# Kernel tuning notes

Measured on AMD Instinct MI355X. Metric: run time of the kernel, lower is better.

Reference implementation:

```python
import jax, jax.numpy as jnp
import numpy as np

B, N = 128, 1024


def setup_inputs() -> dict:
    key = jax.random.key(0)
    k1, k2 = jax.random.split(key)
    vector = jax.random.uniform(k1, (B, N), dtype=jnp.float32)
    interactions = jax.random.normal(k2, (N, N), dtype=jnp.float32)
    return {"vector": vector, "interactions": interactions}


def reference(vector, interactions):
    # x: [B,1,N], y: [B,N,1] -> broadcast dirac delta [B,N,N]
    x = vector[:, None, :]
    y = vector[:, :, None]
    dd = (1.0 - x) * (1.0 - y) + x * y  # [B,N,N]
    dd = jnp.triu(dd)                   # keep upper triangle incl. diagonal
    energy = dd * interactions          # [B,N,N] * [N,N] broadcast
    return energy.reshape(vector.shape[0], -1).sum(axis=1)  # [B]
```

## Files before the change

### kernel.cpp

```cpp
#include <hip/hip_runtime.h>

#define NDIM 1024
#define BDIM 128
#define TS 32
#define NT (NDIM / TS)
#define NTILES (NT * (NT + 1) / 2)

__global__ __launch_bounds__(128) void potts_zero(float* __restrict__ out) {
    out[threadIdx.x] = 0.0f;
}

__global__ __launch_bounds__(256) void potts_tile(
    const float* __restrict__ V,
    const float* __restrict__ W,
    float* __restrict__ out)
{
    const int t = blockIdx.x;
    int ti = 0, rem = t;
    while (rem >= NT - ti) { rem -= NT - ti; ++ti; }
    const int tj = ti + rem;
    const int I0 = ti * TS, J0 = tj * TS;
    const bool diag = (ti == tj);

    __shared__ float wt[TS][36];
    __shared__ float rs[TS];
    __shared__ float red[4][BDIM];

    const int tid = threadIdx.x;
    const int w = tid >> 6;
    const int l = tid & 63;
    const int b0 = l, b1 = l + 64;

    {
        const int r = tid >> 3, c4 = (tid & 7) * 4;
        float4 w4 = *(const float4*)(W + (size_t)(I0 + r) * NDIM + (J0 + c4));
        if (diag) {
            if (c4 + 0 < r) w4.x = 0.0f;
            if (c4 + 1 < r) w4.y = 0.0f;
            if (c4 + 2 < r) w4.z = 0.0f;
            if (c4 + 3 < r) w4.w = 0.0f;
        }
        *(float4*)(&wt[r][c4]) = w4;
        float rsum = (w4.x + w4.y) + (w4.z + w4.w);
        rsum += __shfl_xor(rsum, 1);
        rsum += __shfl_xor(rsum, 2);
        rsum += __shfl_xor(rsum, 4);
        if ((tid & 7) == 0) rs[r] = rsum;
    }

    float4 vj0[8], vj1[8];
    {
        const float* p0 = V + (size_t)b0 * NDIM + J0;
        const float* p1 = V + (size_t)b1 * NDIM + J0;
#pragma unroll
        for (int j4 = 0; j4 < 8; ++j4) {
            vj0[j4] = *(const float4*)(p0 + 4 * j4);
            vj1[j4] = *(const float4*)(p1 + 4 * j4);
        }
    }
    float q0[8], r0[8], q1[8], r1[8];
    {
        const float* p0 = V + (size_t)b0 * NDIM + I0 + w * 8;
        const float* p1 = V + (size_t)b1 * NDIM + I0 + w * 8;
        const float4 a0 = *(const float4*)(p0), a1 = *(const float4*)(p0 + 4);
        const float4 c0 = *(const float4*)(p1), c1 = *(const float4*)(p1 + 4);
        const float va[8] = {a0.x, a0.y, a0.z, a0.w, a1.x, a1.y, a1.z, a1.w};
        const float vc[8] = {c0.x, c0.y, c0.z, c0.w, c1.x, c1.y, c1.z, c1.w};
#pragma unroll
        for (int k = 0; k < 8; ++k) {
            q0[k] = 1.0f - va[k]; r0[k] = 2.0f * va[k] - 1.0f;
            q1[k] = 1.0f - vc[k]; r1[k] = 2.0f * vc[k] - 1.0f;
        }
    }

    __syncthreads();

    float acc0 = 0.0f, acc1 = 0.0f;
#pragma unroll
    for (int k = 0; k < 8; ++k) {
        const float* wrow = &wt[w * 8 + k][0];
        float pa0 = 0.f, pb0 = 0.f, pa1 = 0.f, pb1 = 0.f;
#pragma unroll
        for (int j4 = 0; j4 < 8; j4 += 2) {
            const float4 wa = *(const float4*)(wrow + 4 * j4);
            const float4 wb = *(const float4*)(wrow + 4 * j4 + 4);
            pa0 = fmaf(wa.x, vj0[j4].x, pa0);
            pa0 = fmaf(wa.y, vj0[j4].y, pa0);
            pa0 = fmaf(wa.z, vj0[j4].z, pa0);
            pa0 = fmaf(wa.w, vj0[j4].w, pa0);
            pa1 = fmaf(wa.x, vj1[j4].x, pa1);
            pa1 = fmaf(wa.y, vj1[j4].y, pa1);
            pa1 = fmaf(wa.z, vj1[j4].z, pa1);
            pa1 = fmaf(wa.w, vj1[j4].w, pa1);
            pb0 = fmaf(wb.x, vj0[j4 + 1].x, pb0);
            pb0 = fmaf(wb.y, vj0[j4 + 1].y, pb0);
            pb0 = fmaf(wb.z, vj0[j4 + 1].z, pb0);
            pb0 = fmaf(wb.w, vj0[j4 + 1].w, pb0);
            pb1 = fmaf(wb.x, vj1[j4 + 1].x, pb1);
            pb1 = fmaf(wb.y, vj1[j4 + 1].y, pb1);
            pb1 = fmaf(wb.z, vj1[j4 + 1].z, pb1);
            pb1 = fmaf(wb.w, vj1[j4 + 1].w, pb1);
        }
        const float rsk = rs[w * 8 + k];
        const float rv0 = pa0 + pb0, rv1 = pa1 + pb1;
        acc0 = fmaf(q0[k], rsk, acc0);
        acc0 = fmaf(r0[k], rv0, acc0);
        acc1 = fmaf(q1[k], rsk, acc1);
        acc1 = fmaf(r1[k], rv1, acc1);
    }

    red[w][b0] = acc0;
    red[w][b1] = acc1;
    __syncthreads();
    if (tid < BDIM) {
        const float s = (red[0][tid] + red[1][tid]) + (red[2][tid] + red[3][tid]);
        atomicAdd(&out[tid], s);
    }
}

extern "C" void kernel_launch(void* const* d_in, const int* in_sizes, int n_in,
                              void* d_out, int out_size, void* d_ws, size_t ws_size,
                              hipStream_t stream) {
    const float* V = (const float*)d_in[0];
    const float* W = (const float*)d_in[1];
    float* out = (float*)d_out;

    potts_zero<<<dim3(1), dim3(128), 0, stream>>>(out);
    potts_tile<<<dim3(NTILES), dim3(256), 0, stream>>>(V, W, out);
}
```

Baseline: 77.27 us.

## Stage V tiles through shared memory and replace atomics with two-pass reduction

Each block now loads the 128x32 V slices for both the I and J tiles with coalesced float4 reads, transposes them into padded shared memory, and then has each thread read its per-batch values from LDS. Before, each thread did strided per-row global loads. Per-tile atomicAdd into the output is replaced by writes of per-tile partial sums to workspace, followed by a second deterministic reduction kernel, which also removes the zeroing kernel. The cost is about 33KB of extra shared memory per block, which may lower occupancy, plus an extra kernel and a workspace round-trip.

After: 64.18 us. 1.2x faster.

```diff
diff --git a/kernel.cpp b/kernel.cpp
--- a/kernel.cpp
+++ b/kernel.cpp
@@ -6,14 +6,10 @@
 #define NT (NDIM / TS)
 #define NTILES (NT * (NT + 1) / 2)
 
-__global__ __launch_bounds__(128) void potts_zero(float* __restrict__ out) {
-    out[threadIdx.x] = 0.0f;
-}
-
-__global__ __launch_bounds__(256) void potts_tile(
+__global__ __launch_bounds__(256) void potts_main(
     const float* __restrict__ V,
     const float* __restrict__ W,
-    float* __restrict__ out)
+    float* __restrict__ partial)
 {
     const int t = blockIdx.x;
     int ti = 0, rem = t;
@@ -24,12 +20,13 @@
 
     __shared__ float wt[TS][36];
     __shared__ float rs[TS];
+    __shared__ float vjt[TS][130];
+    __shared__ float vit[TS][130];
     __shared__ float red[4][BDIM];
 
     const int tid = threadIdx.x;
     const int w = tid >> 6;
     const int l = tid & 63;
-    const int b0 = l, b1 = l + 64;
 
     {
         const int r = tid >> 3, c4 = (tid & 7) * 4;
@@ -48,74 +45,89 @@
         if ((tid & 7) == 0) rs[r] = rsum;
     }
 
-    float4 vj0[8], vj1[8];
-    {
-        const float* p0 = V + (size_t)b0 * NDIM + J0;
-        const float* p1 = V + (size_t)b1 * NDIM + J0;
+    for (int it = 0; it < 4; ++it) {
+        const int fid = tid + 256 * it;
+        const int b = fid >> 3, k4 = (fid & 7) * 4;
+        const float4 a = *(const float4*)(V + (size_t)b * NDIM + J0 + k4);
+        vjt[k4 + 0][b] = a.x; vjt[k4 + 1][b] = a.y;
+        vjt[k4 + 2][b] = a.z; vjt[k4 + 3][b] = a.w;
+        const float4 c = *(const float4*)(V + (size_t)b * NDIM + I0 + k4);
+        vit[k4 + 0][b] = c.x; vit[k4 + 1][b] = c.y;
+        vit[k4 + 2][b] = c.z; vit[k4 + 3][b] = c.w;
+    }
+    __syncthreads();
+
+    float vj0[TS], vj1[TS];
 #pragma unroll
-        for (int j4 = 0; j4 < 8; ++j4) {
-            vj0[j4] = *(const float4*)(p0 + 4 * j4);
-            vj1[j4] = *(const float4*)(p1 + 4 * j4);
-        }
+    for (int j = 0; j < TS; ++j) {
+        vj0[j] = vjt[j][l];
+        vj1[j] = vjt[j][l + 64];
     }
-    float q0[8], r0[8], q1[8], r1[8];
-    {
-        const float* p0 = V + (size_t)b0 * NDIM + I0 + w * 8;
-        const float* p1 = V + (size_t)b1 * NDIM + I0 + w * 8;
-        const float4 a0 = *(const float4*)(p0), a1 = *(const float4*)(p0 + 4);
-        const float4 c0 = *(const float4*)(p1), c1 = *(const float4*)(p1 + 4);
-        const float va[8] = {a0.x, a0.y, a0.z, a0.w, a1.x, a1.y, a1.z, a1.w};
-        const float vc[8] = {c0.x, c0.y, c0.z, c0.w, c1.x, c1.y, c1.z, c1.w};
-#pragma unroll
-        for (int k = 0; k < 8; ++k) {
-            q0[k] = 1.0f - va[k]; r0[k] = 2.0f * va[k] - 1.0f;
-            q1[k] = 1.0f - vc[k]; r1[k] = 2.0f * vc[k] - 1.0f;
-        }
-    }
-
-    __syncthreads();
 
     float acc0 = 0.0f, acc1 = 0.0f;
 #pragma unroll
     for (int k = 0; k < 8; ++k) {
-        const float* wrow = &wt[w * 8 + k][0];
-        float pa0 = 0.f, pb0 = 0.f, pa1 = 0.f, pb1 = 0.f;
+        const int i = 8 * w + k;
+        const float vi0 = vit[i][l], vi1 = vit[i][l + 64];
+        const float q0 = 1.0f - vi0, r0 = 2.0f * vi0 - 1.0f;
+        const float q1 = 1.0f - vi1, r1 = 2.0f * vi1 - 1.0f;
+        const float* wrow = &wt[i][0];
+        float za0 = 0.f, zb0 = 0.f, za1 = 0.f, zb1 = 0.f;
 #pragma unroll
         for (int j4 = 0; j4 < 8; j4 += 2) {
             const float4 wa = *(const float4*)(wrow + 4 * j4);
             const float4 wb = *(const float4*)(wrow + 4 * j4 + 4);
-            pa0 = fmaf(wa.x, vj0[j4].x, pa0);
-            pa0 = fmaf(wa.y, vj0[j4].y, pa0);
-            pa0 = fmaf(wa.z, vj0[j4].z, pa0);
-            pa0 = fmaf(wa.w, vj0[j4].w, pa0);
-            pa1 = fmaf(wa.x, vj1[j4].x, pa1);
-            pa1 = fmaf(wa.y, vj1[j4].y, pa1);
-            pa1 = fmaf(wa.z, vj1[j4].z, pa1);
-            pa1 = fmaf(wa.w, vj1[j4].w, pa1);
-            pb0 = fmaf(wb.x, vj0[j4 + 1].x, pb0);
-            pb0 = fmaf(wb.y, vj0[j4 + 1].y, pb0);
-            pb0 = fmaf(wb.z, vj0[j4 + 1].z, pb0);
-            pb0 = fmaf(wb.w, vj0[j4 + 1].w, pb0);
-            pb1 = fmaf(wb.x, vj1[j4 + 1].x, pb1);
-            pb1 = fmaf(wb.y, vj1[j4 + 1].y, pb1);
-            pb1 = fmaf(wb.z, vj1[j4 + 1].z, pb1);
-            pb1 = fmaf(wb.w, vj1[j4 + 1].w, pb1);
+            za0 = fmaf(wa.x, vj0[4 * j4 + 0], za0);
+            za0 = fmaf(wa.y, vj0[4 * j4 + 1], za0);
+            za0 = fmaf(wa.z, vj0[4 * j4 + 2], za0);
+            za0 = fmaf(wa.w, vj0[4 * j4 + 3], za0);
+            za1 = fmaf(wa.x, vj1[4 * j4 + 0], za1);
+            za1 = fmaf(wa.y, vj1[4 * j4 + 1], za1);
+            za1 = fmaf(wa.z, vj1[4 * j4 + 2], za1);
+            za1 = fmaf(wa.w, vj1[4 * j4 + 3], za1);
+            zb0 = fmaf(wb.x, vj0[4 * j4 + 4], zb0);
+            zb0 = fmaf(wb.y, vj0[4 * j4 + 5], zb0);
+            zb0 = fmaf(wb.z, vj0[4 * j4 + 6], zb0);
+            zb0 = fmaf(wb.w, vj0[4 * j4 + 7], zb0);
+            zb1 = fmaf(wb.x, vj1[4 * j4 + 4], zb1);
+            zb1 = fmaf(wb.y, vj1[4 * j4 + 5], zb1);
+            zb1 = fmaf(wb.z, vj1[4 * j4 + 6], zb1);
+            zb1 = fmaf(wb.w, vj1[4 * j4 + 7], zb1);
         }
-        const float rsk = rs[w * 8 + k];
-        const float rv0 = pa0 + pb0, rv1 = pa1 + pb1;
-        acc0 = fmaf(q0[k], rsk, acc0);
-        acc0 = fmaf(r0[k], rv0, acc0);
-        acc1 = fmaf(q1[k], rsk, acc1);
-        acc1 = fmaf(r1[k], rv1, acc1);
+        const float rsk = rs[i];
+        acc0 = fmaf(q0, rsk, acc0);
+        acc0 = fmaf(r0, za0 + zb0, acc0);
+        acc1 = fmaf(q1, rsk, acc1);
+        acc1 = fmaf(r1, za1 + zb1, acc1);
     }
 
-    red[w][b0] = acc0;
-    red[w][b1] = acc1;
+    red[w][l] = acc0;
+    red[w][l + 64] = acc1;
     __syncthreads();
     if (tid < BDIM) {
-        const float s = (red[0][tid] + red[1][tid]) + (red[2][tid] + red[3][tid]);
-        atomicAdd(&out[tid], s);
+        partial[t * BDIM + tid] =
+            (red[0][tid] + red[1][tid]) + (red[2][tid] + red[3][tid]);
     }
+}
+
+__global__ __launch_bounds__(64) void potts_red(
+    const float* __restrict__ partial, float* __restrict__ out)
+{
+    const int b = blockIdx.x;
+    const int lane = threadIdx.x;
+    float a0 = 0.f, a1 = 0.f;
+    int t = lane;
+#pragma unroll 4
+    for (; t + 64 < NTILES; t += 128) {
+        a0 += partial[t * BDIM + b];
+        a1 += partial[(t + 64) * BDIM + b];
+    }
+    if (t < NTILES) a0 += partial[t * BDIM + b];
+    float a = a0 + a1;
+#pragma unroll
+    for (int off = 32; off > 0; off >>= 1)
+        a += __shfl_down(a, off);
+    if (lane == 0) out[b] = a;
 }
 
 extern "C" void kernel_launch(void* const* d_in, const int* in_sizes, int n_in,
@@ -124,7 +136,8 @@
     const float* V = (const float*)d_in[0];
     const float* W = (const float*)d_in[1];
     float* out = (float*)d_out;
+    float* partial = (float*)d_ws;
 
-    potts_zero<<<dim3(1), dim3(128), 0, stream>>>(out);
-    potts_tile<<<dim3(NTILES), dim3(256), 0, stream>>>(V, W, out);
+    potts_main<<<dim3(NTILES), dim3(256), 0, stream>>>(V, W, partial);
+    potts_red<<<dim3(BDIM), dim3(64), 0, stream>>>(partial, out);
 }
```
